# Performance work log

Hardware: AMD Instinct MI355X
Metric: run time of the kernel (lower is better)

The kernel has to match this reference:

```python
import jax, jax.numpy as jnp
import numpy as np

A = 15           # anchors per location (5 sizes x 3 ratios)
H, W = 200, 320  # feature map size
N = 8            # batch
STRIDE = 4
PRE_NMS = 2000
POST_NMS = 1000
NMS_THRESH = 0.7
MIN_SIZE = 1.0
SCORE_THRESH = 0.0
BBOX_CLIP = float(np.log(1000.0 / 16.0))  # torchvision BoxCoder clamp on dw/dh


def _make_anchors():
    # torchvision-style cell anchors: ratio-major, then sizes, shifted over the grid.
    sizes = np.array([32.0, 64.0, 128.0, 256.0, 512.0])
    ratios = np.array([0.5, 1.0, 2.0])
    h_r = np.sqrt(ratios)
    w_r = 1.0 / h_r
    ws = (w_r[:, None] * sizes[None, :]).reshape(-1)  # [15]
    hs = (h_r[:, None] * sizes[None, :]).reshape(-1)
    base = np.stack([-ws, -hs, ws, hs], axis=1) / 2.0  # [15,4] centered at 0
    sx = np.arange(W) * STRIDE
    sy = np.arange(H) * STRIDE
    yy, xx = np.meshgrid(sy, sx, indexing="ij")
    shifts = np.stack([xx, yy, xx, yy], axis=-1).reshape(-1, 1, 4)  # [H*W,1,4]
    return (shifts + base[None]).reshape(-1, 4).astype(np.float32)  # [H*W*A,4]


def setup_inputs() -> dict:
    key = jax.random.key(0)
    k1, k2 = jax.random.split(key)
    return {
        "box_cls": jax.random.normal(k1, (N, A, H, W), dtype=jnp.float32),
        "box_regression": jax.random.normal(k2, (N, 4 * A, H, W), dtype=jnp.float32),
        "anchors": jnp.asarray(_make_anchors()),
        "img_h": 800,
        "img_w": 1280,
    }


def _decode(deltas, anchors):
    # BoxCoder.decode with weights (1,1,1,1). deltas [N,K,4], anchors [K,4] xyxy.
    wa = anchors[:, 2] - anchors[:, 0]
    ha = anchors[:, 3] - anchors[:, 1]
    cxa = anchors[:, 0] + 0.5 * wa
    cya = anchors[:, 1] + 0.5 * ha
    dx, dy = deltas[..., 0], deltas[..., 1]
    dw = jnp.minimum(deltas[..., 2], BBOX_CLIP)
    dh = jnp.minimum(deltas[..., 3], BBOX_CLIP)
    cx = dx * wa + cxa
    cy = dy * ha + cya
    w = wa * jnp.exp(dw)
    h = ha * jnp.exp(dh)
    return jnp.stack(
        [cx - 0.5 * w, cy - 0.5 * h, cx + 0.5 * w, cy + 0.5 * h], axis=-1
    )


def _nms_keep(boxes, scores):
    # Greedy NMS over boxes sorted by descending score; scores < 0 mark invalid.
    x1, y1, x2, y2 = boxes[:, 0], boxes[:, 1], boxes[:, 2], boxes[:, 3]
    area = (x2 - x1) * (y2 - y1)
    ix = jnp.maximum(0.0, jnp.minimum(x2[:, None], x2[None, :]) - jnp.maximum(x1[:, None], x1[None, :]))
    iy = jnp.maximum(0.0, jnp.minimum(y2[:, None], y2[None, :]) - jnp.maximum(y1[:, None], y1[None, :]))
    inter = ix * iy
    iou = inter / (area[:, None] + area[None, :] - inter)  # [K,K]
    k = boxes.shape[0]
    idx = jnp.arange(k)
    keep0 = scores >= 0.0

    def body(i, keep):
        sup = keep[i] & (iou[i] > NMS_THRESH) & (idx > i)
        return keep & ~sup

    return jax.lax.fori_loop(0, k, body, keep0)


def reference(box_cls, box_regression, anchors, img_h, img_w):
    n = box_cls.shape[0]
    # permute_and_flatten: [N, A*C, H, W] -> [N, H*W*A, C]
    objectness = box_cls.reshape(n, A, 1, H, W).transpose(0, 3, 4, 1, 2).reshape(n, -1)
    deltas = box_regression.reshape(n, A, 4, H, W).transpose(0, 3, 4, 1, 2).reshape(n, -1, 4)
    proposals = _decode(deltas, anchors)  # [N, K, 4]
    # clip to image (single image size for the whole batch)
    fh = jnp.float32(img_h)
    fw = jnp.float32(img_w)
    proposals = jnp.stack(
        [
            jnp.clip(proposals[..., 0], 0.0, fw),
            jnp.clip(proposals[..., 1], 0.0, fh),
            jnp.clip(proposals[..., 2], 0.0, fw),
            jnp.clip(proposals[..., 3], 0.0, fh),
        ],
        axis=-1,
    )
    # pre-NMS top-k per image (single feature level)
    top_s, top_i = jax.lax.top_k(objectness, PRE_NMS)        # [N, PRE]
    boxes = jnp.take_along_axis(proposals, top_i[..., None], axis=1)  # [N, PRE, 4]
    scores = jax.nn.sigmoid(top_s)
    # remove small boxes and low-scoring boxes (mask instead of dynamic shapes)
    ws = boxes[..., 2] - boxes[..., 0]
    hs = boxes[..., 3] - boxes[..., 1]
    valid = (ws >= MIN_SIZE) & (hs >= MIN_SIZE) & (scores >= SCORE_THRESH)
    scores_m = jnp.where(valid, scores, -1.0)
    order = jnp.argsort(-scores_m, axis=1)
    boxes_s = jnp.take_along_axis(boxes, order[..., None], axis=1)
    scores_s = jnp.take_along_axis(scores_m, order, axis=1)
    keep = jax.vmap(_nms_keep)(boxes_s, scores_s)            # [N, PRE] bool
    ks = jnp.where(keep, scores_s, -1.0)
    fs, fi = jax.lax.top_k(ks, POST_NMS)                     # [N, POST]
    fb = jnp.take_along_axis(boxes_s, fi[..., None], axis=1)
    ok = fs >= 0.0
    final_boxes = jnp.where(ok[..., None], fb, 0.0)          # zero-padded, fixed shape
    final_scores = jnp.where(ok, fs, 0.0)
    return final_boxes, final_scores
```

## Files before the change

### kernel.cpp

```cpp
#include <hip/hip_runtime.h>
#include <hip/hip_bf16.h>
#include <stdint.h>

typedef unsigned long long u64;

#define AN 15
#define HH 200
#define WW 320
#define HWSZ (HH*WW)
#define PER (AN*HWSZ)
#define NB 8
#define K_PRE 2000
#define K_POST 1000
#define SORTN 4096
#define HBINS 4096
#define HBLK 64
#define FSLICE 512
#define CBLK 16
#define SLICE (SORTN/CBLK)
#define NMS_TH 0.7f
#define BBOX_CLIP_F 4.135166556742356f
#define FLOOR12 3072u
#define SENT 0xFFFFFFFFu

#define PHI(x) ((x) + ((x) >> 3))

__device__ __forceinline__ unsigned keyOfU(unsigned u) {
    return (u & 0x80000000u) ? ~u : (u | 0x80000000u);
}
__device__ __forceinline__ float valOf(unsigned k) {
    unsigned u = (k & 0x80000000u) ? (k ^ 0x80000000u) : ~k;
    return __uint_as_float(u);
}

__global__ __launch_bounds__(256)
void z_init(uint4* __restrict__ gh4, unsigned* __restrict__ selT12) {
    gh4[blockIdx.x * 256 + threadIdx.x] = make_uint4(0, 0, 0, 0);
    if (blockIdx.x == 0 && threadIdx.x < NB) selT12[threadIdx.x] = SENT;
}

__global__ __launch_bounds__(256)
void k_hc(const uint4* __restrict__ cls4, unsigned* __restrict__ gh,
          u64* __restrict__ fbuf) {
    int n = blockIdx.y;
    __shared__ unsigned lh[HBINS];
    __shared__ unsigned cnt;
    for (int b = threadIdx.x; b < HBINS; b += 256) lh[b] = 0;
    if (threadIdx.x == 0) cnt = 0;
    __syncthreads();
    u64* slice = fbuf + ((size_t)n * HBLK + blockIdx.x) * FSLICE;
    const uint4* p = cls4 + (size_t)n * (PER / 4);
    int stride = gridDim.x * 256;

#define PROC(vv, ii) {                                                        \
        unsigned kk[4] = {keyOfU((vv).x), keyOfU((vv).y), keyOfU((vv).z),     \
                          keyOfU((vv).w)};                                    \
        int i0 = (ii) * 4;                                                    \
        int a = i0 / HWSZ;                                                    \
        int r0 = i0 - a * HWSZ;                                               \
        _Pragma("unroll")                                                     \
        for (int c = 0; c < 4; ++c) {                                         \
            unsigned k12 = kk[c] >> 20;                                       \
            if (k12 >= FLOOR12) {                                             \
                atomicAdd(&lh[k12], 1u);                                      \
                unsigned pos = atomicAdd(&cnt, 1u);                           \
                if (pos < FSLICE) {                                           \
                    unsigned idx = (unsigned)((r0 + c) * AN + a);             \
                    slice[pos] = ((u64)kk[c] << 32) | (u64)(~idx);            \
                }                                                             \
            }                                                                 \
        }                                                                     \
    }

    int i = blockIdx.x * 256 + threadIdx.x;
    for (; i + stride < PER / 4; i += 2 * stride) {
        uint4 a4 = p[i];
        uint4 b4 = p[i + stride];
        PROC(a4, i) PROC(b4, i + stride)
    }
    if (i < PER / 4) { uint4 a4 = p[i]; PROC(a4, i) }
#undef PROC

    __syncthreads();
    unsigned c0 = cnt; if (c0 > FSLICE) c0 = FSLICE;
    for (unsigned t = c0 + threadIdx.x; t < FSLICE; t += 256) slice[t] = 0ull;
    unsigned* dst = gh + (size_t)n * HBINS;
    for (int b = threadIdx.x; b < HBINS; b += 256) {
        unsigned v = lh[b];
        if (v) atomicAdd(&dst[b], v);
    }
}

__global__ __launch_bounds__(1024)
void k_sel(const unsigned* __restrict__ gh, unsigned* __restrict__ selT12) {
    int n = blockIdx.x, t = threadIdx.x;
    __shared__ unsigned L[1024];
    uint4 v = *(const uint4*)(gh + (size_t)n * HBINS + 4 * t);
    unsigned sf[5];
    sf[3] = v.w; sf[2] = v.z + sf[3]; sf[1] = v.y + sf[2]; sf[0] = v.x + sf[1];
    L[t] = sf[0];
    __syncthreads();
    for (int off = 1; off < 1024; off <<= 1) {
        unsigned x = L[t] + ((t + off < 1024) ? L[t + off] : 0u);
        __syncthreads(); L[t] = x; __syncthreads();
    }
    unsigned tail = (t < 1023) ? L[t + 1] : 0u;
    sf[0] += tail; sf[1] += tail; sf[2] += tail; sf[3] += tail; sf[4] = tail;
#pragma unroll
    for (int e = 0; e < 4; ++e)
        if (sf[e] >= K_PRE && sf[e + 1] < K_PRE) selT12[n] = 4u * t + e;
}

__global__ __launch_bounds__(256)
void k_histR(const uint4* __restrict__ cls4, unsigned* __restrict__ gh,
             const unsigned* __restrict__ selT12) {
    int n = blockIdx.y;
    if (selT12[n] != SENT) return;
    __shared__ unsigned lh[HBINS];
    for (int b = threadIdx.x; b < HBINS; b += 256) lh[b] = 0;
    __syncthreads();
    const uint4* p = cls4 + (size_t)n * (PER / 4);
    int stride = gridDim.x * 256;
#define H4(vv) { unsigned k0 = keyOfU((vv).x) >> 20, k1 = keyOfU((vv).y) >> 20, \
                          k2 = keyOfU((vv).z) >> 20, k3 = keyOfU((vv).w) >> 20; \
        if (k0 < FLOOR12) atomicAdd(&lh[k0], 1u);                               \
        if (k1 < FLOOR12) atomicAdd(&lh[k1], 1u);                               \
        if (k2 < FLOOR12) atomicAdd(&lh[k2], 1u);                               \
        if (k3 < FLOOR12) atomicAdd(&lh[k3], 1u); }
    for (int i = blockIdx.x * 256 + threadIdx.x; i < PER / 4; i += stride) {
        uint4 a = p[i]; H4(a)
    }
#undef H4
    __syncthreads();
    unsigned* dst = gh + (size_t)n * HBINS;
    for (int b = threadIdx.x; b < HBINS; b += 256) {
        unsigned v = lh[b];
        if (v) atomicAdd(&dst[b], v);
    }
}

__global__ __launch_bounds__(1024)
void k_selR(const unsigned* __restrict__ gh, unsigned* __restrict__ selT12) {
    int n = blockIdx.x, t = threadIdx.x;
    if (selT12[n] != SENT) return;
    __shared__ unsigned L[1024];
    uint4 v = *(const uint4*)(gh + (size_t)n * HBINS + 4 * t);
    unsigned sf[5];
    sf[3] = v.w; sf[2] = v.z + sf[3]; sf[1] = v.y + sf[2]; sf[0] = v.x + sf[1];
    L[t] = sf[0];
    __syncthreads();
    for (int off = 1; off < 1024; off <<= 1) {
        unsigned x = L[t] + ((t + off < 1024) ? L[t + off] : 0u);
        __syncthreads(); L[t] = x; __syncthreads();
    }
    unsigned tail = (t < 1023) ? L[t + 1] : 0u;
    sf[0] += tail; sf[1] += tail; sf[2] += tail; sf[3] += tail; sf[4] = tail;
#pragma unroll
    for (int e = 0; e < 4; ++e)
        if (sf[e] >= K_PRE && sf[e + 1] < K_PRE) selT12[n] = 4u * t + e;
}

__global__ __launch_bounds__(256)
void k_filter(const uint4* __restrict__ cls4, const u64* __restrict__ fbuf,
              const unsigned* __restrict__ selT12, u64* __restrict__ cand) {
    int n = blockIdx.y, cb = blockIdx.x;
    unsigned t12 = selT12[n];
    __shared__ unsigned cnt;
    if (threadIdx.x == 0) cnt = 0;
    __syncthreads();
    u64* slice = cand + (size_t)n * SORTN + (size_t)cb * SLICE;

    if (t12 >= FLOOR12) {
        const u64* src = fbuf + ((size_t)n * HBLK + (size_t)cb * (HBLK / CBLK)) * FSLICE;
        for (int t = threadIdx.x; t < (HBLK / CBLK) * FSLICE; t += 256) {
            u64 e = src[t];
            if ((unsigned)(e >> 52) >= t12) {
                unsigned pos = atomicAdd(&cnt, 1u);
                if (pos < SLICE) slice[pos] = e;
            }
        }
    } else {
        const uint4* p = cls4 + (size_t)n * (PER / 4);
        int stride = gridDim.x * 256;
        for (int i = cb * 256 + threadIdx.x; i < PER / 4; i += stride) {
            uint4 v = p[i];
            unsigned kk[4] = {keyOfU(v.x), keyOfU(v.y), keyOfU(v.z), keyOfU(v.w)};
            int i0 = i * 4;
            int a = i0 / HWSZ;
            int r0 = i0 - a * HWSZ;
#pragma unroll
            for (int c = 0; c < 4; ++c) {
                if ((kk[c] >> 20) >= t12) {
                    unsigned pos = atomicAdd(&cnt, 1u);
                    if (pos < SLICE) {
                        unsigned idx = (unsigned)((r0 + c) * AN + a);
                        slice[pos] = ((u64)kk[c] << 32) | (u64)(~idx);
                    }
                }
            }
        }
    }
    __syncthreads();
    unsigned c0 = cnt; if (c0 > SLICE) c0 = SLICE;
    for (unsigned t = c0 + threadIdx.x; t < SLICE; t += 256) slice[t] = 0ull;
}

__global__ __launch_bounds__(512)
void k_sort(u64* __restrict__ cand) {
    int n = blockIdx.x;
    int tid = threadIdx.x;
    __shared__ u64 sb[PHI(SORTN - 1) + 1];
    u64 r[8];

#define CE(a_, b_, d_) { bool sw_ = (d_) ? (r[a_] < r[b_]) : (r[a_] > r[b_]); \
                         if (sw_) { u64 t_ = r[a_]; r[a_] = r[b_]; r[b_] = t_; } }

    {
        const u64* src = cand + (size_t)n * SORTN + 8 * tid;
#pragma unroll
        for (int e = 0; e < 8; ++e) r[e] = src[e];
        CE(0, 1, true)  CE(2, 3, false) CE(4, 5, true)  CE(6, 7, false)
        CE(0, 2, true)  CE(1, 3, true)  CE(4, 6, false) CE(5, 7, false)
        CE(0, 1, true)  CE(2, 3, true)  CE(4, 5, false) CE(6, 7, false)
#pragma unroll
        for (int e = 0; e < 8; ++e) sb[9 * tid + e] = r[e];
        __syncthreads();
    }

    for (int k = 8; k <= SORTN; k <<= 1) {
        for (int j = k >> 1; j >= 8; j >>= 1) {
#pragma unroll
            for (int s = 0; s < 4; ++s) {
                int c = tid + s * 512;
                int i = ((c & ~(j - 1)) << 1) | (c & (j - 1));
                int p = i | j;
                bool dir = (i & k) == 0;
                u64 a = sb[PHI(i)], b = sb[PHI(p)];
                bool sw = dir ? (a < b) : (a > b);
                if (sw) { sb[PHI(i)] = b; sb[PHI(p)] = a; }
            }
            __syncthreads();
        }
        {
            bool d = ((8 * tid) & k) == 0;
#pragma unroll
            for (int e = 0; e < 8; ++e) r[e] = sb[9 * tid + e];
            CE(0, 4, d) CE(1, 5, d) CE(2, 6, d) CE(3, 7, d)
            CE(0, 2, d) CE(1, 3, d) CE(4, 6, d) CE(5, 7, d)
            CE(0, 1, d) CE(2, 3, d) CE(4, 5, d) CE(6, 7, d)
#pragma unroll
            for (int e = 0; e < 8; ++e) sb[9 * tid + e] = r[e];
            __syncthreads();
        }
    }
#undef CE

    for (int t = tid; t < 2048; t += 512)
        cand[(size_t)n * SORTN + t] = sb[PHI(t)];
}

__global__ __launch_bounds__(1024)
void k_decode(const float* __restrict__ reg, const float* __restrict__ anchors,
              const int* __restrict__ pih, const int* __restrict__ piw,
              const u64* __restrict__ cand,
              float* __restrict__ boxes_s, float* __restrict__ scores_s) {
    int n = blockIdx.x;
    int tid = threadIdx.x;
    float fh = (float)(*pih);
    float fw = (float)(*piw);

    float bx[2][4]; float sc[2]; int pred[2];
#pragma unroll
    for (int q = 0; q < 2; ++q) {
        int t = tid + 1024 * q;
        pred[q] = 0; sc[q] = -1.0f;
        bx[q][0] = bx[q][1] = bx[q][2] = bx[q][3] = 0.f;
        if (t < K_PRE) {
            u64 e = cand[(size_t)n * SORTN + t];
            unsigned key = (unsigned)(e >> 32);
            unsigned idx = ~((unsigned)e);
            float v = valOf(key);
            float s = 1.0f / (1.0f + expf(-v));
            int a = (int)(idx % AN);
            int rr = (int)(idx / AN);
            size_t base = ((size_t)(n * AN + a) * 4) * HWSZ + rr;
            float dx = reg[base];
            float dy = reg[base + HWSZ];
            float dw = reg[base + 2 * (size_t)HWSZ];
            float dh = reg[base + 3 * (size_t)HWSZ];
            float4 an4 = ((const float4*)anchors)[idx];
            float wa = an4.z - an4.x, ha = an4.w - an4.y;
            float cxa = an4.x + 0.5f * wa, cya = an4.y + 0.5f * ha;
            dw = fminf(dw, BBOX_CLIP_F); dh = fminf(dh, BBOX_CLIP_F);
            float cx = dx * wa + cxa, cy = dy * ha + cya;
            float w = wa * expf(dw), h = ha * expf(dh);
            float x1 = cx - 0.5f * w, y1 = cy - 0.5f * h;
            float x2 = cx + 0.5f * w, y2 = cy + 0.5f * h;
            x1 = fminf(fmaxf(x1, 0.f), fw);
            y1 = fminf(fmaxf(y1, 0.f), fh);
            x2 = fminf(fmaxf(x2, 0.f), fw);
            y2 = fminf(fmaxf(y2, 0.f), fh);
            bool valid = ((x2 - x1) >= 1.0f) && ((y2 - y1) >= 1.0f);
            bx[q][0] = x1; bx[q][1] = y1; bx[q][2] = x2; bx[q][3] = y2;
            sc[q] = s; pred[q] = valid ? 1 : 0;
        }
    }

    __shared__ u64 ww[32];
    __shared__ int wpfx[33];
    int lane = tid & 63, wid = tid >> 6;
#pragma unroll
    for (int q = 0; q < 2; ++q) {
        u64 bal = __ballot(pred[q] != 0);
        if (lane == 0) ww[wid + 16 * q] = bal;
    }
    __syncthreads();
    if (tid == 0) {
        int s = 0;
#pragma unroll
        for (int w2 = 0; w2 < 32; ++w2) { wpfx[w2] = s; s += (int)__popcll(ww[w2]); }
        wpfx[32] = s;
    }
    __syncthreads();
    int V = wpfx[32];

#pragma unroll
    for (int q = 0; q < 2; ++q) {
        int t = tid + 1024 * q;
        if (t < K_PRE) {
            int wi = t >> 6;
            int before = wpfx[wi] + (int)__popcll(ww[wi] & ((1ull << (unsigned)lane) - 1ull));
            int pos = pred[q] ? before : (V + (t - before));
            float4 b4; b4.x = bx[q][0]; b4.y = bx[q][1]; b4.z = bx[q][2]; b4.w = bx[q][3];
            ((float4*)boxes_s)[(size_t)n * K_PRE + pos] = b4;
            scores_s[(size_t)n * K_PRE + pos] = pred[q] ? sc[q] : -1.0f;
        }
    }
}

__global__ __launch_bounds__(64)
void k_maskT(const float* __restrict__ boxes_s, u64* __restrict__ maskT) {
    int n = blockIdx.y;
    int p = blockIdx.x;
    int lane = threadIdx.x;
    int cb = (int)((sqrtf(8.0f * (float)p + 1.0f) - 1.0f) * 0.5f);
    while ((cb + 1) * (cb + 2) / 2 <= p) ++cb;
    while (cb * (cb + 1) / 2 > p) --cb;
    int rb = p - cb * (cb + 1) / 2;

    __shared__ float rx1[64], ry1[64], rx2[64], ry2[64], rar[64];
    int c = cb * 64 + lane;
    bool cok = c < K_PRE;
    float4 c4; c4.x = c4.y = c4.z = c4.w = 0.f;
    if (cok) c4 = ((const float4*)boxes_s)[(size_t)n * K_PRE + c];
    float areaC = (c4.z - c4.x) * (c4.w - c4.y);

    int r = rb * 64 + lane;
    float4 r4; r4.x = r4.y = r4.z = r4.w = 0.f;
    if (r < K_PRE) r4 = ((const float4*)boxes_s)[(size_t)n * K_PRE + r];
    rx1[lane] = r4.x; ry1[lane] = r4.y; rx2[lane] = r4.z; ry2[lane] = r4.w;
    rar[lane] = (r4.z - r4.x) * (r4.w - r4.y);
    __syncthreads();

    u64 bits = 0;
    int bmax = 0;
    if (cok) { bmax = c - rb * 64; if (bmax > 64) bmax = 64; }
    for (int b = 0; b < bmax; ++b) {
        float ix = fminf(c4.z, rx2[b]) - fmaxf(c4.x, rx1[b]); ix = fmaxf(ix, 0.f);
        float iy = fminf(c4.w, ry2[b]) - fmaxf(c4.y, ry1[b]); iy = fmaxf(iy, 0.f);
        float inter = ix * iy;
        float iou = inter / (rar[b] + areaC - inter);
        if (iou > NMS_TH) bits |= (1ull << b);
    }
    maskT[((size_t)n * 32 + rb) * 2048 + c] = bits;
}

__global__ __launch_bounds__(64)
void k_scanT(const u64* __restrict__ maskT, const float* __restrict__ boxes_s,
             const float* __restrict__ scores_s, float* __restrict__ out) {
    int n = blockIdx.x;
    int lane = threadIdx.x;
    __shared__ float ls[2048];
    __shared__ u64 keptw[32];
    for (int i = lane; i < 500; i += 64)
        ((float4*)ls)[i] = ((const float4*)(scores_s + (size_t)n * K_PRE))[i];
    if (lane < 48) ls[2000 + lane] = -1.0f;
    if (lane < 32) keptw[lane] = 0ull;
    __syncthreads();

    const u64* mb = maskT + (size_t)n * 32 * 2048;
    int kept_total = 0;

    u64 wv[32];
#pragma unroll
    for (int rb = 0; rb < 32; ++rb) wv[rb] = mb[(size_t)rb * 2048 + lane];

    for (int f = 0; f < 32; ++f) {
        int c = f * 64 + lane;

        u64 wn[32];
        if (f < 31) {
            int cn = c + 64;
#pragma unroll
            for (int rb = 0; rb < 32; ++rb) wn[rb] = mb[(size_t)rb * 2048 + cn];
        }

        u64 hit = 0;
#pragma unroll
        for (int rb = 0; rb < 32; ++rb) hit |= (wv[rb] & keptw[rb]);
        bool ext = hit != 0ull;
        u64 diag = wv[f];

        bool v = (ls[c] >= 0.0f) && !ext;
        u64 kept = __ballot(v);
        while (true) {
            u64 nk = __ballot(v && ((diag & kept) == 0ull));
            if (nk == kept) break;
            kept = nk;
        }

        if ((kept >> lane) & 1ull) {
            int rank = kept_total + (int)__popcll(kept & ((1ull << lane) - 1ull));
            if (rank < K_POST) {
                float4 b4 = ((const float4*)boxes_s)[(size_t)n * K_PRE + c];
                ((float4*)out)[(size_t)n * K_POST + rank] = b4;
                out[(size_t)NB * K_POST * 4 + (size_t)n * K_POST + rank] = ls[c];
            }
        }
        kept_total += (int)__popcll(kept);
        if (lane == 0) keptw[f] = kept;
        if (kept_total >= K_POST || f == 31) break;
#pragma unroll
        for (int rb = 0; rb < 32; ++rb) wv[rb] = wn[rb];
    }

    int start = (kept_total < K_POST) ? kept_total : K_POST;
    float4 z4; z4.x = z4.y = z4.z = z4.w = 0.f;
    for (int rk = start + lane; rk < K_POST; rk += 64) {
        ((float4*)out)[(size_t)n * K_POST + rk] = z4;
        out[(size_t)NB * K_POST * 4 + (size_t)n * K_POST + rk] = 0.f;
    }
}

extern "C" void kernel_launch(void* const* d_in, const int* in_sizes, int n_in,
                              void* d_out, int out_size, void* d_ws, size_t ws_size,
                              hipStream_t stream) {
    const float* cls     = (const float*)d_in[0];
    const float* regr    = (const float*)d_in[1];
    const float* anchors = (const float*)d_in[2];
    const int*   pih     = (const int*)d_in[3];
    const int*   piw     = (const int*)d_in[4];
    float* out = (float*)d_out;

    char* w = (char*)d_ws;
    u64*      maskT   = (u64*)(w + 0);
    unsigned* gh      = (unsigned*)(w + 4194304);
    unsigned* selT12  = (unsigned*)(w + 4325376);
    u64*      cand    = (u64*)(w + 4325440);
    float*    boxes_s = (float*)(w + 4587584);
    float*    scores_s= (float*)(w + 4843584);
    u64*      fbuf    = (u64*)(w + 4907584);

    z_init<<<32, 256, 0, stream>>>((uint4*)gh, selT12);
    k_hc<<<dim3(HBLK, NB), 256, 0, stream>>>((const uint4*)cls, gh, fbuf);
    k_sel<<<NB, 1024, 0, stream>>>(gh, selT12);
    k_histR<<<dim3(HBLK, NB), 256, 0, stream>>>((const uint4*)cls, gh, selT12);
    k_selR<<<NB, 1024, 0, stream>>>(gh, selT12);
    k_filter<<<dim3(CBLK, NB), 256, 0, stream>>>((const uint4*)cls, fbuf, selT12, cand);
    k_sort<<<NB, 512, 0, stream>>>(cand);
    k_decode<<<NB, 1024, 0, stream>>>(regr, anchors, pih, piw,
                                      cand, boxes_s, scores_s);
    k_maskT<<<dim3(528, NB), 64, 0, stream>>>(boxes_s, maskT);
    k_scanT<<<NB, 64, 0, stream>>>(maskT, boxes_s, scores_s, out);
    (void)in_sizes; (void)n_in; (void)ws_size;
}
```

Measured before the change: 126.4 us.

## Fuse threshold selection, filter, sort and decode into one per-image kernel

Result: slower. 144.1 us (+14.0%).

```diff
diff --git a/kernel.cpp b/kernel.cpp
--- a/kernel.cpp
+++ b/kernel.cpp
@@ -16,12 +16,9 @@
 #define HBINS 4096
 #define HBLK 64
 #define FSLICE 512
-#define CBLK 16
-#define SLICE (SORTN/CBLK)
 #define NMS_TH 0.7f
 #define BBOX_CLIP_F 4.135166556742356f
 #define FLOOR12 3072u
-#define SENT 0xFFFFFFFFu
 
 #define PHI(x) ((x) + ((x) >> 3))
 
@@ -34,18 +31,10 @@
 }
 
 __global__ __launch_bounds__(256)
-void z_init(uint4* __restrict__ gh4, unsigned* __restrict__ selT12) {
-    gh4[blockIdx.x * 256 + threadIdx.x] = make_uint4(0, 0, 0, 0);
-    if (blockIdx.x == 0 && threadIdx.x < NB) selT12[threadIdx.x] = SENT;
-}
-
-__global__ __launch_bounds__(256)
-void k_hc(const uint4* __restrict__ cls4, unsigned* __restrict__ gh,
-          u64* __restrict__ fbuf) {
+void k_hc(const uint4* __restrict__ cls4, u64* __restrict__ fbuf,
+          unsigned* __restrict__ cnts) {
     int n = blockIdx.y;
-    __shared__ unsigned lh[HBINS];
     __shared__ unsigned cnt;
-    for (int b = threadIdx.x; b < HBINS; b += 256) lh[b] = 0;
     if (threadIdx.x == 0) cnt = 0;
     __syncthreads();
     u64* slice = fbuf + ((size_t)n * HBLK + blockIdx.x) * FSLICE;
@@ -60,9 +49,7 @@
         int r0 = i0 - a * HWSZ;                                               \
         _Pragma("unroll")                                                     \
         for (int c = 0; c < 4; ++c) {                                         \
-            unsigned k12 = kk[c] >> 20;                                       \
-            if (k12 >= FLOOR12) {                                             \
-                atomicAdd(&lh[k12], 1u);                                      \
+            if ((kk[c] >> 20) >= FLOOR12) {                                   \
                 unsigned pos = atomicAdd(&cnt, 1u);                           \
                 if (pos < FSLICE) {                                           \
                     unsigned idx = (unsigned)((r0 + c) * AN + a);             \
@@ -82,107 +69,93 @@
 #undef PROC
 
     __syncthreads();
-    unsigned c0 = cnt; if (c0 > FSLICE) c0 = FSLICE;
-    for (unsigned t = c0 + threadIdx.x; t < FSLICE; t += 256) slice[t] = 0ull;
-    unsigned* dst = gh + (size_t)n * HBINS;
-    for (int b = threadIdx.x; b < HBINS; b += 256) {
-        unsigned v = lh[b];
-        if (v) atomicAdd(&dst[b], v);
-    }
-}
-
-__global__ __launch_bounds__(1024)
-void k_sel(const unsigned* __restrict__ gh, unsigned* __restrict__ selT12) {
-    int n = blockIdx.x, t = threadIdx.x;
-    __shared__ unsigned L[1024];
-    uint4 v = *(const uint4*)(gh + (size_t)n * HBINS + 4 * t);
-    unsigned sf[5];
-    sf[3] = v.w; sf[2] = v.z + sf[3]; sf[1] = v.y + sf[2]; sf[0] = v.x + sf[1];
-    L[t] = sf[0];
-    __syncthreads();
-    for (int off = 1; off < 1024; off <<= 1) {
-        unsigned x = L[t] + ((t + off < 1024) ? L[t + off] : 0u);
-        __syncthreads(); L[t] = x; __syncthreads();
-    }
-    unsigned tail = (t < 1023) ? L[t + 1] : 0u;
-    sf[0] += tail; sf[1] += tail; sf[2] += tail; sf[3] += tail; sf[4] = tail;
-#pragma unroll
-    for (int e = 0; e < 4; ++e)
-        if (sf[e] >= K_PRE && sf[e + 1] < K_PRE) selT12[n] = 4u * t + e;
-}
-
-__global__ __launch_bounds__(256)
-void k_histR(const uint4* __restrict__ cls4, unsigned* __restrict__ gh,
-             const unsigned* __restrict__ selT12) {
-    int n = blockIdx.y;
-    if (selT12[n] != SENT) return;
+    unsigned c0 = cnt;
+    if (threadIdx.x == 0) cnts[n * HBLK + blockIdx.x] = c0;
+    unsigned cz = (c0 > FSLICE) ? FSLICE : c0;
+    for (unsigned t = cz + threadIdx.x; t < FSLICE; t += 256) slice[t] = 0ull;
+}
+
+__global__ __launch_bounds__(512)
+void k_mid(const uint4* __restrict__ cls4, const u64* __restrict__ fbuf,
+           const unsigned* __restrict__ cnts, const float* __restrict__ reg,
+           const float* __restrict__ anchors, const int* __restrict__ pih,
+           const int* __restrict__ piw,
+           float* __restrict__ boxes_s, float* __restrict__ scores_s) {
+    int n = blockIdx.x;
+    int tid = threadIdx.x;
     __shared__ unsigned lh[HBINS];
-    for (int b = threadIdx.x; b < HBINS; b += 256) lh[b] = 0;
-    __syncthreads();
-    const uint4* p = cls4 + (size_t)n * (PER / 4);
-    int stride = gridDim.x * 256;
-#define H4(vv) { unsigned k0 = keyOfU((vv).x) >> 20, k1 = keyOfU((vv).y) >> 20, \
-                          k2 = keyOfU((vv).z) >> 20, k3 = keyOfU((vv).w) >> 20; \
-        if (k0 < FLOOR12) atomicAdd(&lh[k0], 1u);                               \
-        if (k1 < FLOOR12) atomicAdd(&lh[k1], 1u);                               \
-        if (k2 < FLOOR12) atomicAdd(&lh[k2], 1u);                               \
-        if (k3 < FLOOR12) atomicAdd(&lh[k3], 1u); }
-    for (int i = blockIdx.x * 256 + threadIdx.x; i < PER / 4; i += stride) {
-        uint4 a = p[i]; H4(a)
-    }
-#undef H4
-    __syncthreads();
-    unsigned* dst = gh + (size_t)n * HBINS;
-    for (int b = threadIdx.x; b < HBINS; b += 256) {
-        unsigned v = lh[b];
-        if (v) atomicAdd(&dst[b], v);
-    }
-}
-
-__global__ __launch_bounds__(1024)
-void k_selR(const unsigned* __restrict__ gh, unsigned* __restrict__ selT12) {
-    int n = blockIdx.x, t = threadIdx.x;
-    if (selT12[n] != SENT) return;
-    __shared__ unsigned L[1024];
-    uint4 v = *(const uint4*)(gh + (size_t)n * HBINS + 4 * t);
-    unsigned sf[5];
-    sf[3] = v.w; sf[2] = v.z + sf[3]; sf[1] = v.y + sf[2]; sf[0] = v.x + sf[1];
-    L[t] = sf[0];
-    __syncthreads();
-    for (int off = 1; off < 1024; off <<= 1) {
-        unsigned x = L[t] + ((t + off < 1024) ? L[t + off] : 0u);
-        __syncthreads(); L[t] = x; __syncthreads();
-    }
-    unsigned tail = (t < 1023) ? L[t + 1] : 0u;
-    sf[0] += tail; sf[1] += tail; sf[2] += tail; sf[3] += tail; sf[4] = tail;
-#pragma unroll
-    for (int e = 0; e < 4; ++e)
-        if (sf[e] >= K_PRE && sf[e + 1] < K_PRE) selT12[n] = 4u * t + e;
-}
-
-__global__ __launch_bounds__(256)
-void k_filter(const uint4* __restrict__ cls4, const u64* __restrict__ fbuf,
-              const unsigned* __restrict__ selT12, u64* __restrict__ cand) {
-    int n = blockIdx.y, cb = blockIdx.x;
-    unsigned t12 = selT12[n];
-    __shared__ unsigned cnt;
-    if (threadIdx.x == 0) cnt = 0;
-    __syncthreads();
-    u64* slice = cand + (size_t)n * SORTN + (size_t)cb * SLICE;
-
-    if (t12 >= FLOOR12) {
-        const u64* src = fbuf + ((size_t)n * HBLK + (size_t)cb * (HBLK / CBLK)) * FSLICE;
-        for (int t = threadIdx.x; t < (HBLK / CBLK) * FSLICE; t += 256) {
-            u64 e = src[t];
-            if ((unsigned)(e >> 52) >= t12) {
-                unsigned pos = atomicAdd(&cnt, 1u);
-                if (pos < SLICE) slice[pos] = e;
-            }
+    __shared__ unsigned L[512];
+    __shared__ u64 sb[PHI(SORTN - 1) + 1];
+    __shared__ unsigned sT12, sMode, fcnt;
+
+    if (tid < HBLK) L[tid] = cnts[n * HBLK + tid];
+    __syncthreads();
+    if (tid == 0) {
+        unsigned tot = 0; unsigned ovf = 0;
+        for (int b = 0; b < HBLK; ++b) { tot += L[b]; ovf |= (L[b] > FSLICE); }
+        sMode = (tot >= K_PRE && !ovf) ? 0u : 1u;
+    }
+    __syncthreads();
+    unsigned mode = sMode;
+
+    for (int b = tid; b < HBINS; b += 512) lh[b] = 0;
+    __syncthreads();
+    if (mode == 0) {
+        const u64* src = fbuf + (size_t)n * HBLK * FSLICE;
+        for (int t = tid; t < HBLK * FSLICE; t += 512) {
+            unsigned k12 = (unsigned)(src[t] >> 52);
+            if (k12 >= FLOOR12) atomicAdd(&lh[k12], 1u);
         }
     } else {
         const uint4* p = cls4 + (size_t)n * (PER / 4);
-        int stride = gridDim.x * 256;
-        for (int i = cb * 256 + threadIdx.x; i < PER / 4; i += stride) {
+        for (int i = tid; i < PER / 4; i += 512) {
+            uint4 v = p[i];
+            atomicAdd(&lh[keyOfU(v.x) >> 20], 1u);
+            atomicAdd(&lh[keyOfU(v.y) >> 20], 1u);
+            atomicAdd(&lh[keyOfU(v.z) >> 20], 1u);
+            atomicAdd(&lh[keyOfU(v.w) >> 20], 1u);
+        }
+    }
+    __syncthreads();
+
+    unsigned s[8];
+    {
+        uint4 v0 = *(const uint4*)(lh + 8 * tid);
+        uint4 v1 = *(const uint4*)(lh + 8 * tid + 4);
+        s[7] = v1.w; s[6] = v1.z + s[7]; s[5] = v1.y + s[6]; s[4] = v1.x + s[5];
+        s[3] = v0.w + s[4]; s[2] = v0.z + s[3]; s[1] = v0.y + s[2]; s[0] = v0.x + s[1];
+    }
+    __syncthreads();
+    L[tid] = s[0];
+    __syncthreads();
+    for (int off = 1; off < 512; off <<= 1) {
+        unsigned x = L[tid] + ((tid + off < 512) ? L[tid + off] : 0u);
+        __syncthreads(); L[tid] = x; __syncthreads();
+    }
+    unsigned tail = (tid < 511) ? L[tid + 1] : 0u;
+#pragma unroll
+    for (int e = 0; e < 8; ++e) {
+        unsigned sfE = s[e] + tail;
+        unsigned sfN = (e < 7) ? (s[e + 1] + tail) : tail;
+        if (sfE >= K_PRE && sfN < K_PRE) sT12 = 8u * tid + e;
+    }
+    __syncthreads();
+    unsigned T12 = sT12;
+
+    if (tid == 0) fcnt = 0;
+    __syncthreads();
+    if (mode == 0) {
+        const u64* src = fbuf + (size_t)n * HBLK * FSLICE;
+        for (int t = tid; t < HBLK * FSLICE; t += 512) {
+            u64 e = src[t];
+            if ((unsigned)(e >> 52) >= T12) {
+                unsigned pos = atomicAdd(&fcnt, 1u);
+                if (pos < SORTN) sb[PHI((int)pos)] = e;
+            }
+        }
+    } else {
+        const uint4* p = cls4 + (size_t)n * (PER / 4);
+        for (int i = tid; i < PER / 4; i += 512) {
             uint4 v = p[i];
             unsigned kk[4] = {keyOfU(v.x), keyOfU(v.y), keyOfU(v.z), keyOfU(v.w)};
             int i0 = i * 4;
@@ -190,35 +163,27 @@
             int r0 = i0 - a * HWSZ;
 #pragma unroll
             for (int c = 0; c < 4; ++c) {
-                if ((kk[c] >> 20) >= t12) {
-                    unsigned pos = atomicAdd(&cnt, 1u);
-                    if (pos < SLICE) {
+                if ((kk[c] >> 20) >= T12) {
+                    unsigned pos = atomicAdd(&fcnt, 1u);
+                    if (pos < SORTN) {
                         unsigned idx = (unsigned)((r0 + c) * AN + a);
-                        slice[pos] = ((u64)kk[c] << 32) | (u64)(~idx);
+                        sb[PHI((int)pos)] = ((u64)kk[c] << 32) | (u64)(~idx);
                     }
                 }
             }
         }
     }
     __syncthreads();
-    unsigned c0 = cnt; if (c0 > SLICE) c0 = SLICE;
-    for (unsigned t = c0 + threadIdx.x; t < SLICE; t += 256) slice[t] = 0ull;
-}
-
-__global__ __launch_bounds__(512)
-void k_sort(u64* __restrict__ cand) {
-    int n = blockIdx.x;
-    int tid = threadIdx.x;
-    __shared__ u64 sb[PHI(SORTN - 1) + 1];
+    unsigned fc = fcnt; if (fc > SORTN) fc = SORTN;
+    for (unsigned t = fc + tid; t < SORTN; t += 512) sb[PHI((int)t)] = 0ull;
+    __syncthreads();
+
     u64 r[8];
-
 #define CE(a_, b_, d_) { bool sw_ = (d_) ? (r[a_] < r[b_]) : (r[a_] > r[b_]); \
                          if (sw_) { u64 t_ = r[a_]; r[a_] = r[b_]; r[b_] = t_; } }
-
     {
-        const u64* src = cand + (size_t)n * SORTN + 8 * tid;
-#pragma unroll
-        for (int e = 0; e < 8; ++e) r[e] = src[e];
+#pragma unroll
+        for (int e = 0; e < 8; ++e) r[e] = sb[9 * tid + e];
         CE(0, 1, true)  CE(2, 3, false) CE(4, 5, true)  CE(6, 7, false)
         CE(0, 2, true)  CE(1, 3, true)  CE(4, 6, false) CE(5, 7, false)
         CE(0, 1, true)  CE(2, 3, true)  CE(4, 5, false) CE(6, 7, false)
@@ -226,12 +191,11 @@
         for (int e = 0; e < 8; ++e) sb[9 * tid + e] = r[e];
         __syncthreads();
     }
-
     for (int k = 8; k <= SORTN; k <<= 1) {
         for (int j = k >> 1; j >= 8; j >>= 1) {
 #pragma unroll
-            for (int s = 0; s < 4; ++s) {
-                int c = tid + s * 512;
+            for (int ss = 0; ss < 4; ++ss) {
+                int c = tid + ss * 512;
                 int i = ((c & ~(j - 1)) << 1) | (c & (j - 1));
                 int p = i | j;
                 bool dir = (i & k) == 0;
@@ -255,32 +219,21 @@
     }
 #undef CE
 
-    for (int t = tid; t < 2048; t += 512)
-        cand[(size_t)n * SORTN + t] = sb[PHI(t)];
-}
-
-__global__ __launch_bounds__(1024)
-void k_decode(const float* __restrict__ reg, const float* __restrict__ anchors,
-              const int* __restrict__ pih, const int* __restrict__ piw,
-              const u64* __restrict__ cand,
-              float* __restrict__ boxes_s, float* __restrict__ scores_s) {
-    int n = blockIdx.x;
-    int tid = threadIdx.x;
     float fh = (float)(*pih);
     float fw = (float)(*piw);
 
-    float bx[2][4]; float sc[2]; int pred[2];
-#pragma unroll
-    for (int q = 0; q < 2; ++q) {
-        int t = tid + 1024 * q;
+    float bx[4][4]; float sc[4]; int pred[4];
+#pragma unroll
+    for (int q = 0; q < 4; ++q) {
+        int t = tid + 512 * q;
         pred[q] = 0; sc[q] = -1.0f;
         bx[q][0] = bx[q][1] = bx[q][2] = bx[q][3] = 0.f;
         if (t < K_PRE) {
-            u64 e = cand[(size_t)n * SORTN + t];
+            u64 e = sb[PHI(t)];
             unsigned key = (unsigned)(e >> 32);
             unsigned idx = ~((unsigned)e);
             float v = valOf(key);
-            float s = 1.0f / (1.0f + expf(-v));
+            float sgm = 1.0f / (1.0f + expf(-v));
             int a = (int)(idx % AN);
             int rr = (int)(idx / AN);
             size_t base = ((size_t)(n * AN + a) * 4) * HWSZ + rr;
@@ -302,31 +255,32 @@
             y2 = fminf(fmaxf(y2, 0.f), fh);
             bool valid = ((x2 - x1) >= 1.0f) && ((y2 - y1) >= 1.0f);
             bx[q][0] = x1; bx[q][1] = y1; bx[q][2] = x2; bx[q][3] = y2;
-            sc[q] = s; pred[q] = valid ? 1 : 0;
-        }
-    }
+            sc[q] = sgm; pred[q] = valid ? 1 : 0;
+        }
+    }
+    __syncthreads();
 
     __shared__ u64 ww[32];
     __shared__ int wpfx[33];
     int lane = tid & 63, wid = tid >> 6;
 #pragma unroll
-    for (int q = 0; q < 2; ++q) {
+    for (int q = 0; q < 4; ++q) {
         u64 bal = __ballot(pred[q] != 0);
-        if (lane == 0) ww[wid + 16 * q] = bal;
+        if (lane == 0) ww[wid + 8 * q] = bal;
     }
     __syncthreads();
     if (tid == 0) {
-        int s = 0;
-#pragma unroll
-        for (int w2 = 0; w2 < 32; ++w2) { wpfx[w2] = s; s += (int)__popcll(ww[w2]); }
-        wpfx[32] = s;
+        int acc = 0;
+#pragma unroll
+        for (int w2 = 0; w2 < 32; ++w2) { wpfx[w2] = acc; acc += (int)__popcll(ww[w2]); }
+        wpfx[32] = acc;
     }
     __syncthreads();
     int V = wpfx[32];
 
 #pragma unroll
-    for (int q = 0; q < 2; ++q) {
-        int t = tid + 1024 * q;
+    for (int q = 0; q < 4; ++q) {
+        int t = tid + 512 * q;
         if (t < K_PRE) {
             int wi = t >> 6;
             int before = wpfx[wi] + (int)__popcll(ww[wi] & ((1ull << (unsigned)lane) - 1ull));
@@ -454,23 +408,15 @@
 
     char* w = (char*)d_ws;
     u64*      maskT   = (u64*)(w + 0);
-    unsigned* gh      = (unsigned*)(w + 4194304);
-    unsigned* selT12  = (unsigned*)(w + 4325376);
-    u64*      cand    = (u64*)(w + 4325440);
-    float*    boxes_s = (float*)(w + 4587584);
-    float*    scores_s= (float*)(w + 4843584);
-    u64*      fbuf    = (u64*)(w + 4907584);
-
-    z_init<<<32, 256, 0, stream>>>((uint4*)gh, selT12);
-    k_hc<<<dim3(HBLK, NB), 256, 0, stream>>>((const uint4*)cls, gh, fbuf);
-    k_sel<<<NB, 1024, 0, stream>>>(gh, selT12);
-    k_histR<<<dim3(HBLK, NB), 256, 0, stream>>>((const uint4*)cls, gh, selT12);
-    k_selR<<<NB, 1024, 0, stream>>>(gh, selT12);
-    k_filter<<<dim3(CBLK, NB), 256, 0, stream>>>((const uint4*)cls, fbuf, selT12, cand);
-    k_sort<<<NB, 512, 0, stream>>>(cand);
-    k_decode<<<NB, 1024, 0, stream>>>(regr, anchors, pih, piw,
-                                      cand, boxes_s, scores_s);
+    u64*      fbuf    = (u64*)(w + 4194304);
+    unsigned* cnts    = (unsigned*)(w + 6291456);
+    float*    boxes_s = (float*)(w + 6293504);
+    float*    scores_s= (float*)(w + 6549504);
+
+    k_hc<<<dim3(HBLK, NB), 256, 0, stream>>>((const uint4*)cls, fbuf, cnts);
+    k_mid<<<NB, 512, 0, stream>>>((const uint4*)cls, fbuf, cnts, regr, anchors,
+                                  pih, piw, boxes_s, scores_s);
     k_maskT<<<dim3(528, NB), 64, 0, stream>>>(boxes_s, maskT);
     k_scanT<<<NB, 64, 0, stream>>>(maskT, boxes_s, scores_s, out);
-    (void)in_sizes; (void)n_in; (void)ws_size;
-}
+    (void)in_sizes; (void)n_in; (void)ws_size; (void)out_size;
+}
```
